# Kernel tuning notes

Measured on AMD Instinct MI355X. Metric: run time of the kernel, lower is better.

The kernel has to match this reference:

```python
import jax, jax.numpy as jnp
import numpy as np

N_QUBITS = 4
DEPTH = 2
B = 2048
IMG = 28
NUM_CLASSES = 2


def _apply_ry(state, theta, wire):
    # state: [N,2,2,2,2] complex64; RY(theta) on given wire (axis 1+wire)
    c = jnp.cos(theta / 2).astype(state.dtype)
    s = jnp.sin(theta / 2).astype(state.dtype)
    a0 = jnp.take(state, 0, axis=1 + wire)
    a1 = jnp.take(state, 1, axis=1 + wire)
    return jnp.stack([c * a0 - s * a1, s * a0 + c * a1], axis=1 + wire)


def _apply_crz(state, theta, control, target):
    # diagonal gate: multiply amplitudes with control bit = 1 by exp(+/- i theta/2)
    sc = [1, 1, 1, 1, 1]; sc[1 + control] = 2
    st = [1, 1, 1, 1, 1]; st[1 + target] = 2
    bc = jnp.arange(2).reshape(sc)
    bt = jnp.arange(2, dtype=jnp.float32).reshape(st)
    phase = jnp.exp((1j * (theta / 2) * (2.0 * bt - 1.0)).astype(state.dtype))
    return state * jnp.where(bc == 1, phase, jnp.ones((), state.dtype))


def _circuit(angles, ry_theta, crz_theta):
    # angles: [N,4]. Encoder resets to |0000> then RY(angle_k) on wire k ->
    # product state with per-wire amplitudes [cos(a/2), sin(a/2)].
    amp = jnp.stack([jnp.cos(angles / 2), jnp.sin(angles / 2)], axis=-1).astype(jnp.complex64)  # [N,4,2]
    state = jnp.einsum('na,nb,nc,nd->nabcd', amp[:, 0], amp[:, 1], amp[:, 2], amp[:, 3])
    for _ in range(DEPTH):
        for i in range(N_QUBITS):
            state = _apply_crz(state, crz_theta, i, (i + 1) % N_QUBITS)
        for j in range(N_QUBITS):
            state = _apply_ry(state, ry_theta, j)
    probs = jnp.real(state * jnp.conj(state))  # [N,2,2,2,2]
    sign = jnp.array([1.0, -1.0], dtype=probs.dtype)
    zs = [jnp.einsum('nabcd,' + 'abcd'[w] + '->n', probs, sign) for w in range(N_QUBITS)]
    return jnp.stack(zs, axis=-1)  # [N,4] PauliZ expectations, wire order 0..3


def _forward(x, ry_theta, crz_theta, fc1_w, fc1_b, fc2_w, fc2_b):
    ry_theta = ry_theta.reshape(())
    crz_theta = crz_theta.reshape(())
    b = x.shape[0]
    h = x.shape[2] // 2
    w = x.shape[3] // 2
    # stride-2 2x2 patches, row-major patch order, (di,dj) pixel order inside patch
    p = x.reshape(b, h, 2, w, 2).transpose(0, 1, 3, 2, 4).reshape(b * h * w, 4)
    z = _circuit(p, ry_theta, crz_theta).reshape(b, h * w * N_QUBITS)  # [B,784]
    hid = jax.nn.relu(z @ fc1_w.T + fc1_b)
    return hid @ fc2_w.T + fc2_b


def setup_inputs() -> dict:
    key = jax.random.key(0)
    ks = jax.random.split(key, 7)
    feat = N_QUBITS * (IMG // 2) * (IMG // 2)  # 784
    return {
        'x': jax.random.normal(ks[0], (B, 1, IMG, IMG), dtype=jnp.float32),
        'ry_theta': jax.random.normal(ks[1], (1,), dtype=jnp.float32),
        'crz_theta': jax.random.normal(ks[2], (1,), dtype=jnp.float32),
        'fc1_w': jax.random.normal(ks[3], (20, feat), dtype=jnp.float32) / np.sqrt(feat),
        'fc1_b': jax.random.normal(ks[4], (20,), dtype=jnp.float32) * 0.01,
        'fc2_w': jax.random.normal(ks[5], (NUM_CLASSES, 20), dtype=jnp.float32) / np.sqrt(20.0),
        'fc2_b': jax.random.normal(ks[6], (NUM_CLASSES,), dtype=jnp.float32) * 0.01,
    }


def reference(x, ry_theta, crz_theta, fc1_w, fc1_b, fc2_w, fc2_b):
    return _forward(x, ry_theta, crz_theta, fc1_w, fc1_b, fc2_w, fc2_b)
```

## Files before the change

kernel.cpp:

```cpp
#include <hip/hip_runtime.h>
#include <math.h>

#define NQ     4
#define IMGD   28
#define HP     14
#define NPATCH 196
#define BATCH  2048
#define FEAT   784
#define HID    20
#define NCLS   2
#define BTHR   320

__device__ __constant__ int d_ktab[16] = {0,-1,-1,0,-1,-2,0,1,-1,0,-2,1,0,1,1,4};


#define RYP(i,j)                                                    \
    { const float t0r = cr##i, t1r = cr##j;                         \
      const float t0i = ci##i, t1i = ci##j;                         \
      cr##i = cy * t0r - sy * t1r;  cr##j = sy * t0r + cy * t1r;    \
      ci##i = cy * t0i - sy * t1i;  ci##j = sy * t0i + cy * t1i; }

#define RY_LAYER()                                                  \
     RYP(0,8)  RYP(1,9)  RYP(2,10) RYP(3,11)     \
                       RYP(4,12) RYP(5,13) RYP(6,14) RYP(7,15)     \
     RYP(0,4)  RYP(1,5)  RYP(2,6)  RYP(3,7)      \
                       RYP(8,12) RYP(9,13) RYP(10,14) RYP(11,15)   \
     RYP(0,2)  RYP(1,3)  RYP(4,6)  RYP(5,7)      \
                       RYP(8,10) RYP(9,11) RYP(12,14) RYP(13,15)   \
     RYP(0,1)  RYP(2,3)  RYP(4,5)  RYP(6,7)      \
                       RYP(8,9)  RYP(10,11) RYP(12,13) RYP(14,15)

#define CRZC(i, c_, s_)                                             \
    { const float nr = cr##i * (c_) - ci##i * (s_);                 \
      ci##i = cr##i * (s_) + ci##i * (c_);  cr##i = nr; }

__global__ __launch_bounds__(256) void patch_z_kernel(
    const float* __restrict__ x,
    const float* __restrict__ ry_theta,
    const float* __restrict__ crz_theta,
    float* __restrict__ z)
{
    const int p  = blockIdx.x * 256 + threadIdx.x;
    const int b  = p / NPATCH;
    const int r  = p - b * NPATCH;
    const int ph = r / HP, pw = r - ph * HP;

    const float hcrz = 0.5f * crz_theta[0];
    const float c1 = __cosf(hcrz), s1 = __sinf(hcrz);
    const float c2 = c1 * c1 - s1 * s1, s2 = 2.f * c1 * s1;
    const float c4 = c2 * c2 - s2 * s2, s4 = 2.f * c2 * s2;
    const float hry = 0.5f * ry_theta[0];
    const float cy = __cosf(hry), sy = __sinf(hry);

    const float* xb = x + (size_t)b * (IMGD * IMGD);
    const float2 p0 = *(const float2*)(xb + (2 * ph)     * IMGD + 2 * pw);
    const float2 p1 = *(const float2*)(xb + (2 * ph + 1) * IMGD + 2 * pw);

    const float h0 = 0.5f * p0.x, h1 = 0.5f * p0.y;
    const float h2 = 0.5f * p1.x, h3 = 0.5f * p1.y;
    const float A0 = __cosf(h0), S0  = __sinf(h0);
    const float A1 = __cosf(h1), S1v = __sinf(h1);
    const float A2 = __cosf(h2), S2v = __sinf(h2);
    const float A3 = __cosf(h3), S3v = __sinf(h3);

    const float q00 = A0 * A1,  q01 = A0 * S1v, q10 = S0 * A1,  q11 = S0 * S1v;
    const float r00 = A2 * A3,  r01 = A2 * S3v, r10 = S2v * A3, r11 = S2v * S3v;
    float cr0  = q00 * r00, cr1  = q00 * r01, cr2  = q00 * r10, cr3  = q00 * r11;
    float cr4  = q01 * r00, cr5  = q01 * r01, cr6  = q01 * r10, cr7  = q01 * r11;
    float cr8  = q10 * r00, cr9  = q10 * r01, cr10 = q10 * r10, cr11 = q10 * r11;
    float cr12 = q11 * r00, cr13 = q11 * r01, cr14 = q11 * r10, cr15 = q11 * r11;

    float ci0 = 0.f, ci3 = 0.f, ci6 = 0.f, ci9 = 0.f, ci12 = 0.f;
    float ci1  = -cr1  * s1;  cr1  *= c1;
    float ci2  = -cr2  * s1;  cr2  *= c1;
    float ci4  = -cr4  * s1;  cr4  *= c1;
    float ci5  = -cr5  * s2;  cr5  *= c2;
    float ci7  =  cr7  * s1;  cr7  *= c1;
    float ci8  = -cr8  * s1;  cr8  *= c1;
    float ci10 = -cr10 * s2;  cr10 *= c2;
    float ci11 =  cr11 * s1;  cr11 *= c1;
    float ci13 =  cr13 * s1;  cr13 *= c1;
    float ci14 =  cr14 * s1;  cr14 *= c1;
    float ci15 =  cr15 * s4;  cr15 *= c4;

    RY_LAYER()

    CRZC(1,  c1, -s1)  CRZC(2,  c1, -s1)  CRZC(4,  c1, -s1)  CRZC(8,  c1, -s1)
    CRZC(5,  c2, -s2)  CRZC(10, c2, -s2)
    CRZC(7,  c1,  s1)  CRZC(11, c1,  s1)  CRZC(13, c1,  s1)  CRZC(14, c1,  s1)
    CRZC(15, c4,  s4)

    RY_LAYER()

#define PROB(i) const float pp##i = cr##i * cr##i + ci##i * ci##i;
    PROB(0) PROB(1) PROB(2) PROB(3) PROB(4) PROB(5) PROB(6) PROB(7)
    PROB(8) PROB(9) PROB(10) PROB(11) PROB(12) PROB(13) PROB(14) PROB(15)
#undef PROB
    const float t01 = pp0 + pp1,   t23 = pp2 + pp3;
    const float t45 = pp4 + pp5,   t67 = pp6 + pp7;
    const float t89 = pp8 + pp9,   tab = pp10 + pp11;
    const float tcd = pp12 + pp13, tef = pp14 + pp15;
    const float u0 = t01 + t23, u1 = t45 + t67, u2 = t89 + tab, u3 = tcd + tef;
    const float z0 = (u0 + u1) - (u2 + u3);
    const float z1 = (u0 + u2) - (u1 + u3);
    const float z2 = (t01 - t23) + (t45 - t67) + (t89 - tab) + (tcd - tef);
    const float z3 = ((pp0 - pp1) + (pp2 - pp3)) + ((pp4 - pp5) + (pp6 - pp7))
                   + ((pp8 - pp9) + (pp10 - pp11)) + ((pp12 - pp13) + (pp14 - pp15));

    *((float4*)&z[(size_t)p * 4]) = make_float4(z0, z1, z2, z3);
}

__global__ __launch_bounds__(BTHR) void fc_kernel(
    const float* __restrict__ z,
    const float* __restrict__ fc1_w,
    const float* __restrict__ fc1_b,
    const float* __restrict__ fc2_w,
    const float* __restrict__ fc2_b,
    float* __restrict__ out)
{
    __shared__ float zs[FEAT];
    __shared__ float hid_s[HID];

    const int tid = threadIdx.x;
    const int b   = blockIdx.x;

    if (tid < NPATCH)
        ((float4*)zs)[tid] = ((const float4*)(z + (size_t)b * FEAT))[tid];
    __syncthreads();

    const int g = tid >> 4;
    const int l = tid & 15;
    const float* wrow = fc1_w + g * FEAT;

    float4 a4 = make_float4(0.f, 0.f, 0.f, 0.f);
    const float4* z4 = (const float4*)zs;
    const float4* w4 = (const float4*)wrow;
    #pragma unroll
    for (int i = 0; i < 12; ++i) {
        const int f4 = l + (i << 4);
        const float4 zz = z4[f4];
        const float4 ww = w4[f4];
        a4.x += zz.x * ww.x;  a4.y += zz.y * ww.y;
        a4.z += zz.z * ww.z;  a4.w += zz.w * ww.w;
    }
    float acc = (a4.x + a4.y) + (a4.z + a4.w);
    acc += zs[768 + l] * wrow[768 + l];

    acc += __shfl_xor(acc, 1, 16);
    acc += __shfl_xor(acc, 2, 16);
    acc += __shfl_xor(acc, 4, 16);
    acc += __shfl_xor(acc, 8, 16);
    if (l == 0) hid_s[g] = acc + fc1_b[g];
    __syncthreads();

    if (tid < NCLS) {
        float o = fc2_b[tid];
        #pragma unroll
        for (int h = 0; h < HID; ++h)
            o += fmaxf(hid_s[h], 0.f) * fc2_w[tid * HID + h];
        out[b * NCLS + tid] = o;
    }
}

__global__ __launch_bounds__(256) void fused_qnn_kernel(
    const float* __restrict__ x, const float* __restrict__ ry_theta,
    const float* __restrict__ crz_theta, const float* __restrict__ fc1_w,
    const float* __restrict__ fc1_b, const float* __restrict__ fc2_w,
    const float* __restrict__ fc2_b, float* __restrict__ out)
{
    __shared__ float zs[FEAT];
    __shared__ float pc_s[16], ps_s[16];
    __shared__ float rycs[2];
    __shared__ float hid_s[HID];

    const int tid = threadIdx.x;
    const int b   = blockIdx.x;

    if (tid < 16) {
        float sv, cv;
        sincosf(0.5f * crz_theta[0] * (float)d_ktab[tid], &sv, &cv);
        pc_s[tid] = cv; ps_s[tid] = sv;
    } else if (tid == 16) {
        float sv, cv;
        sincosf(0.5f * ry_theta[0], &sv, &cv);
        rycs[0] = cv; rycs[1] = sv;
    }
    __syncthreads();

    if (tid < NPATCH) {
        const int ph = tid / HP, pw = tid % HP;
        const float* xb = x + (size_t)b * (IMGD * IMGD);
        const float2 p0 = *(const float2*)(xb + (2 * ph)     * IMGD + 2 * pw);
        const float2 p1 = *(const float2*)(xb + (2 * ph + 1) * IMGD + 2 * pw);
        const float ang[4] = {p0.x, p0.y, p1.x, p1.y};

        float Ac[4], As[4];
        #pragma unroll
        for (int k = 0; k < 4; ++k) { As[k] = __sinf(0.5f * ang[k]); Ac[k] = __cosf(0.5f * ang[k]); }

        float cr[16], ci[16];
        #pragma unroll
        for (int i = 0; i < 16; ++i) {
            cr[i] = ((i & 8) ? As[0] : Ac[0]) * ((i & 4) ? As[1] : Ac[1]) *
                    ((i & 2) ? As[2] : Ac[2]) * ((i & 1) ? As[3] : Ac[3]);
            ci[i] = 0.0f;
        }

        const float c = rycs[0], s = rycs[1];
        #pragma unroll
        for (int layer = 0; layer < 2; ++layer) {
            #pragma unroll
            for (int i = 0; i < 16; ++i) {
                const float pr = pc_s[i], pi = ps_s[i];
                const float nr = cr[i] * pr - ci[i] * pi;
                const float ni = cr[i] * pi + ci[i] * pr;
                cr[i] = nr; ci[i] = ni;
            }
            #pragma unroll
            for (int w = 0; w < 4; ++w) {
                const int m = 8 >> w;
                #pragma unroll
                for (int i = 0; i < 16; ++i) {
                    if (i & m) continue;
                    const int j = i | m;
                    const float a0r = cr[i], a1r = cr[j];
                    const float a0i = ci[i], a1i = ci[j];
                    cr[i] = c * a0r - s * a1r;
                    cr[j] = s * a0r + c * a1r;
                    ci[i] = c * a0i - s * a1i;
                    ci[j] = s * a0i + c * a1i;
                }
            }
        }

        float z0 = 0.f, z1 = 0.f, z2 = 0.f, z3 = 0.f;
        #pragma unroll
        for (int i = 0; i < 16; ++i) {
            const float pr = cr[i] * cr[i] + ci[i] * ci[i];
            z0 += (i & 8) ? -pr : pr;
            z1 += (i & 4) ? -pr : pr;
            z2 += (i & 2) ? -pr : pr;
            z3 += (i & 1) ? -pr : pr;
        }
        *((float4*)&zs[tid * 4]) = make_float4(z0, z1, z2, z3);
    }
    __syncthreads();

    const int wave = tid >> 6;
    const int lane = tid & 63;
    #pragma unroll
    for (int hh = 0; hh < 5; ++hh) {
        const int h = wave * 5 + hh;
        const float* wrow = fc1_w + h * FEAT;
        float acc = 0.f;
        #pragma unroll
        for (int f = lane; f < FEAT; f += 64)
            acc += zs[f] * wrow[f];
        #pragma unroll
        for (int off = 32; off > 0; off >>= 1)
            acc += __shfl_down(acc, off, 64);
        if (lane == 0) hid_s[h] = acc + fc1_b[h];
    }
    __syncthreads();

    if (tid < NCLS) {
        float acc = fc2_b[tid];
        #pragma unroll
        for (int h = 0; h < HID; ++h)
            acc += fmaxf(hid_s[h], 0.f) * fc2_w[tid * HID + h];
        out[b * NCLS + tid] = acc;
    }
}

extern "C" void kernel_launch(void* const* d_in, const int* in_sizes, int n_in,
                              void* d_out, int out_size, void* d_ws, size_t ws_size,
                              hipStream_t stream) {
    const float* x         = (const float*)d_in[0];
    const float* ry_theta  = (const float*)d_in[1];
    const float* crz_theta = (const float*)d_in[2];
    const float* fc1_w     = (const float*)d_in[3];
    const float* fc1_b     = (const float*)d_in[4];
    const float* fc2_w     = (const float*)d_in[5];
    const float* fc2_b     = (const float*)d_in[6];
    float* out = (float*)d_out;

    const size_t z_bytes = (size_t)BATCH * FEAT * sizeof(float);
    if (ws_size >= z_bytes) {
        float* z = (float*)d_ws;
        patch_z_kernel<<<(BATCH * NPATCH) / 256, 256, 0, stream>>>(
            x, ry_theta, crz_theta, z);
        fc_kernel<<<BATCH, BTHR, 0, stream>>>(z, fc1_w, fc1_b, fc2_w, fc2_b, out);
    } else {
        fused_qnn_kernel<<<BATCH, 256, 0, stream>>>(
            x, ry_theta, crz_theta, fc1_w, fc1_b, fc2_w, fc2_b, out);
    }
}
```

Measured before the change: 85.58 us.

## Fuse patch circuit and FC layers into one kernel per image

Replaces the two-kernel path (patch circuit writing z to workspace, then FC kernel reading it) with a single kernel per batch image. The optimized unrolled circuit code writes Z expectations straight into shared memory, and the 256-thread block then computes the 20 hidden units in two passes of 16-lane groups. This removes the global round trip of the 6.4 MB z buffer and one kernel launch. In exchange, only 196 of 256 threads do circuit work and the block is less parallel per image.

```diff
diff --git a/kernel.cpp b/kernel.cpp
--- a/kernel.cpp
+++ b/kernel.cpp
@@ -9,9 +9,6 @@
 #define FEAT   784
 #define HID    20
 #define NCLS   2
-#define BTHR   320
-
-__device__ __constant__ int d_ktab[16] = {0,-1,-1,0,-1,-2,0,1,-1,0,-2,1,0,1,1,4};
 
 
 #define RYP(i,j)                                                    \
@@ -34,84 +31,10 @@
     { const float nr = cr##i * (c_) - ci##i * (s_);                 \
       ci##i = cr##i * (s_) + ci##i * (c_);  cr##i = nr; }
 
-__global__ __launch_bounds__(256) void patch_z_kernel(
+__global__ __launch_bounds__(256) void fused_qnn_kernel(
     const float* __restrict__ x,
     const float* __restrict__ ry_theta,
     const float* __restrict__ crz_theta,
-    float* __restrict__ z)
-{
-    const int p  = blockIdx.x * 256 + threadIdx.x;
-    const int b  = p / NPATCH;
-    const int r  = p - b * NPATCH;
-    const int ph = r / HP, pw = r - ph * HP;
-
-    const float hcrz = 0.5f * crz_theta[0];
-    const float c1 = __cosf(hcrz), s1 = __sinf(hcrz);
-    const float c2 = c1 * c1 - s1 * s1, s2 = 2.f * c1 * s1;
-    const float c4 = c2 * c2 - s2 * s2, s4 = 2.f * c2 * s2;
-    const float hry = 0.5f * ry_theta[0];
-    const float cy = __cosf(hry), sy = __sinf(hry);
-
-    const float* xb = x + (size_t)b * (IMGD * IMGD);
-    const float2 p0 = *(const float2*)(xb + (2 * ph)     * IMGD + 2 * pw);
-    const float2 p1 = *(const float2*)(xb + (2 * ph + 1) * IMGD + 2 * pw);
-
-    const float h0 = 0.5f * p0.x, h1 = 0.5f * p0.y;
-    const float h2 = 0.5f * p1.x, h3 = 0.5f * p1.y;
-    const float A0 = __cosf(h0), S0  = __sinf(h0);
-    const float A1 = __cosf(h1), S1v = __sinf(h1);
-    const float A2 = __cosf(h2), S2v = __sinf(h2);
-    const float A3 = __cosf(h3), S3v = __sinf(h3);
-
-    const float q00 = A0 * A1,  q01 = A0 * S1v, q10 = S0 * A1,  q11 = S0 * S1v;
-    const float r00 = A2 * A3,  r01 = A2 * S3v, r10 = S2v * A3, r11 = S2v * S3v;
-    float cr0  = q00 * r00, cr1  = q00 * r01, cr2  = q00 * r10, cr3  = q00 * r11;
-    float cr4  = q01 * r00, cr5  = q01 * r01, cr6  = q01 * r10, cr7  = q01 * r11;
-    float cr8  = q10 * r00, cr9  = q10 * r01, cr10 = q10 * r10, cr11 = q10 * r11;
-    float cr12 = q11 * r00, cr13 = q11 * r01, cr14 = q11 * r10, cr15 = q11 * r11;
-
-    float ci0 = 0.f, ci3 = 0.f, ci6 = 0.f, ci9 = 0.f, ci12 = 0.f;
-    float ci1  = -cr1  * s1;  cr1  *= c1;
-    float ci2  = -cr2  * s1;  cr2  *= c1;
-    float ci4  = -cr4  * s1;  cr4  *= c1;
-    float ci5  = -cr5  * s2;  cr5  *= c2;
-    float ci7  =  cr7  * s1;  cr7  *= c1;
-    float ci8  = -cr8  * s1;  cr8  *= c1;
-    float ci10 = -cr10 * s2;  cr10 *= c2;
-    float ci11 =  cr11 * s1;  cr11 *= c1;
-    float ci13 =  cr13 * s1;  cr13 *= c1;
-    float ci14 =  cr14 * s1;  cr14 *= c1;
-    float ci15 =  cr15 * s4;  cr15 *= c4;
-
-    RY_LAYER()
-
-    CRZC(1,  c1, -s1)  CRZC(2,  c1, -s1)  CRZC(4,  c1, -s1)  CRZC(8,  c1, -s1)
-    CRZC(5,  c2, -s2)  CRZC(10, c2, -s2)
-    CRZC(7,  c1,  s1)  CRZC(11, c1,  s1)  CRZC(13, c1,  s1)  CRZC(14, c1,  s1)
-    CRZC(15, c4,  s4)
-
-    RY_LAYER()
-
-#define PROB(i) const float pp##i = cr##i * cr##i + ci##i * ci##i;
-    PROB(0) PROB(1) PROB(2) PROB(3) PROB(4) PROB(5) PROB(6) PROB(7)
-    PROB(8) PROB(9) PROB(10) PROB(11) PROB(12) PROB(13) PROB(14) PROB(15)
-#undef PROB
-    const float t01 = pp0 + pp1,   t23 = pp2 + pp3;
-    const float t45 = pp4 + pp5,   t67 = pp6 + pp7;
-    const float t89 = pp8 + pp9,   tab = pp10 + pp11;
-    const float tcd = pp12 + pp13, tef = pp14 + pp15;
-    const float u0 = t01 + t23, u1 = t45 + t67, u2 = t89 + tab, u3 = tcd + tef;
-    const float z0 = (u0 + u1) - (u2 + u3);
-    const float z1 = (u0 + u2) - (u1 + u3);
-    const float z2 = (t01 - t23) + (t45 - t67) + (t89 - tab) + (tcd - tef);
-    const float z3 = ((pp0 - pp1) + (pp2 - pp3)) + ((pp4 - pp5) + (pp6 - pp7))
-                   + ((pp8 - pp9) + (pp10 - pp11)) + ((pp12 - pp13) + (pp14 - pp15));
-
-    *((float4*)&z[(size_t)p * 4]) = make_float4(z0, z1, z2, z3);
-}
-
-__global__ __launch_bounds__(BTHR) void fc_kernel(
-    const float* __restrict__ z,
     const float* __restrict__ fc1_w,
     const float* __restrict__ fc1_b,
     const float* __restrict__ fc2_w,
@@ -124,33 +47,103 @@
     const int tid = threadIdx.x;
     const int b   = blockIdx.x;
 
-    if (tid < NPATCH)
-        ((float4*)zs)[tid] = ((const float4*)(z + (size_t)b * FEAT))[tid];
+    const float hcrz = 0.5f * crz_theta[0];
+    const float c1 = __cosf(hcrz), s1 = __sinf(hcrz);
+    const float c2 = c1 * c1 - s1 * s1, s2 = 2.f * c1 * s1;
+    const float c4 = c2 * c2 - s2 * s2, s4 = 2.f * c2 * s2;
+    const float hry = 0.5f * ry_theta[0];
+    const float cy = __cosf(hry), sy = __sinf(hry);
+
+    if (tid < NPATCH) {
+        const int ph = tid / HP, pw = tid - ph * HP;
+        const float* xb = x + (size_t)b * (IMGD * IMGD);
+        const float2 p0 = *(const float2*)(xb + (2 * ph)     * IMGD + 2 * pw);
+        const float2 p1 = *(const float2*)(xb + (2 * ph + 1) * IMGD + 2 * pw);
+
+        const float h0 = 0.5f * p0.x, h1 = 0.5f * p0.y;
+        const float h2 = 0.5f * p1.x, h3 = 0.5f * p1.y;
+        const float A0 = __cosf(h0), S0  = __sinf(h0);
+        const float A1 = __cosf(h1), S1v = __sinf(h1);
+        const float A2 = __cosf(h2), S2v = __sinf(h2);
+        const float A3 = __cosf(h3), S3v = __sinf(h3);
+
+        const float q00 = A0 * A1,  q01 = A0 * S1v, q10 = S0 * A1,  q11 = S0 * S1v;
+        const float r00 = A2 * A3,  r01 = A2 * S3v, r10 = S2v * A3, r11 = S2v * S3v;
+        float cr0  = q00 * r00, cr1  = q00 * r01, cr2  = q00 * r10, cr3  = q00 * r11;
+        float cr4  = q01 * r00, cr5  = q01 * r01, cr6  = q01 * r10, cr7  = q01 * r11;
+        float cr8  = q10 * r00, cr9  = q10 * r01, cr10 = q10 * r10, cr11 = q10 * r11;
+        float cr12 = q11 * r00, cr13 = q11 * r01, cr14 = q11 * r10, cr15 = q11 * r11;
+
+        float ci0 = 0.f, ci3 = 0.f, ci6 = 0.f, ci9 = 0.f, ci12 = 0.f;
+        float ci1  = -cr1  * s1;  cr1  *= c1;
+        float ci2  = -cr2  * s1;  cr2  *= c1;
+        float ci4  = -cr4  * s1;  cr4  *= c1;
+        float ci5  = -cr5  * s2;  cr5  *= c2;
+        float ci7  =  cr7  * s1;  cr7  *= c1;
+        float ci8  = -cr8  * s1;  cr8  *= c1;
+        float ci10 = -cr10 * s2;  cr10 *= c2;
+        float ci11 =  cr11 * s1;  cr11 *= c1;
+        float ci13 =  cr13 * s1;  cr13 *= c1;
+        float ci14 =  cr14 * s1;  cr14 *= c1;
+        float ci15 =  cr15 * s4;  cr15 *= c4;
+
+        RY_LAYER()
+
+        CRZC(1,  c1, -s1)  CRZC(2,  c1, -s1)  CRZC(4,  c1, -s1)  CRZC(8,  c1, -s1)
+        CRZC(5,  c2, -s2)  CRZC(10, c2, -s2)
+        CRZC(7,  c1,  s1)  CRZC(11, c1,  s1)  CRZC(13, c1,  s1)  CRZC(14, c1,  s1)
+        CRZC(15, c4,  s4)
+
+        RY_LAYER()
+
+#define PROB(i) const float pp##i = cr##i * cr##i + ci##i * ci##i;
+        PROB(0) PROB(1) PROB(2) PROB(3) PROB(4) PROB(5) PROB(6) PROB(7)
+        PROB(8) PROB(9) PROB(10) PROB(11) PROB(12) PROB(13) PROB(14) PROB(15)
+#undef PROB
+        const float t01 = pp0 + pp1,   t23 = pp2 + pp3;
+        const float t45 = pp4 + pp5,   t67 = pp6 + pp7;
+        const float t89 = pp8 + pp9,   tab = pp10 + pp11;
+        const float tcd = pp12 + pp13, tef = pp14 + pp15;
+        const float u0 = t01 + t23, u1 = t45 + t67, u2 = t89 + tab, u3 = tcd + tef;
+        const float z0 = (u0 + u1) - (u2 + u3);
+        const float z1 = (u0 + u2) - (u1 + u3);
+        const float z2 = (t01 - t23) + (t45 - t67) + (t89 - tab) + (tcd - tef);
+        const float z3 = ((pp0 - pp1) + (pp2 - pp3)) + ((pp4 - pp5) + (pp6 - pp7))
+                       + ((pp8 - pp9) + (pp10 - pp11)) + ((pp12 - pp13) + (pp14 - pp15));
+
+        *((float4*)&zs[tid * 4]) = make_float4(z0, z1, z2, z3);
+    }
     __syncthreads();
 
     const int g = tid >> 4;
     const int l = tid & 15;
-    const float* wrow = fc1_w + g * FEAT;
+    const float4* z4 = (const float4*)zs;
 
-    float4 a4 = make_float4(0.f, 0.f, 0.f, 0.f);
-    const float4* z4 = (const float4*)zs;
-    const float4* w4 = (const float4*)wrow;
     #pragma unroll
-    for (int i = 0; i < 12; ++i) {
-        const int f4 = l + (i << 4);
-        const float4 zz = z4[f4];
-        const float4 ww = w4[f4];
-        a4.x += zz.x * ww.x;  a4.y += zz.y * ww.y;
-        a4.z += zz.z * ww.z;  a4.w += zz.w * ww.w;
+    for (int pass = 0; pass < 2; ++pass) {
+        const int h = (pass == 0) ? g : (16 + g);
+        if (pass == 1 && g >= 4) break;
+        const float* wrow = fc1_w + h * FEAT;
+        const float4* w4 = (const float4*)wrow;
+
+        float4 a4 = make_float4(0.f, 0.f, 0.f, 0.f);
+        #pragma unroll
+        for (int i = 0; i < 12; ++i) {
+            const int f4 = l + (i << 4);
+            const float4 zz = z4[f4];
+            const float4 ww = w4[f4];
+            a4.x += zz.x * ww.x;  a4.y += zz.y * ww.y;
+            a4.z += zz.z * ww.z;  a4.w += zz.w * ww.w;
+        }
+        float acc = (a4.x + a4.y) + (a4.z + a4.w);
+        acc += zs[768 + l] * wrow[768 + l];
+
+        acc += __shfl_xor(acc, 1, 16);
+        acc += __shfl_xor(acc, 2, 16);
+        acc += __shfl_xor(acc, 4, 16);
+        acc += __shfl_xor(acc, 8, 16);
+        if (l == 0) hid_s[h] = acc + fc1_b[h];
     }
-    float acc = (a4.x + a4.y) + (a4.z + a4.w);
-    acc += zs[768 + l] * wrow[768 + l];
-
-    acc += __shfl_xor(acc, 1, 16);
-    acc += __shfl_xor(acc, 2, 16);
-    acc += __shfl_xor(acc, 4, 16);
-    acc += __shfl_xor(acc, 8, 16);
-    if (l == 0) hid_s[g] = acc + fc1_b[g];
     __syncthreads();
 
     if (tid < NCLS) {
@@ -159,116 +152,6 @@
         for (int h = 0; h < HID; ++h)
             o += fmaxf(hid_s[h], 0.f) * fc2_w[tid * HID + h];
         out[b * NCLS + tid] = o;
-    }
-}
-
-__global__ __launch_bounds__(256) void fused_qnn_kernel(
-    const float* __restrict__ x, const float* __restrict__ ry_theta,
-    const float* __restrict__ crz_theta, const float* __restrict__ fc1_w,
-    const float* __restrict__ fc1_b, const float* __restrict__ fc2_w,
-    const float* __restrict__ fc2_b, float* __restrict__ out)
-{
-    __shared__ float zs[FEAT];
-    __shared__ float pc_s[16], ps_s[16];
-    __shared__ float rycs[2];
-    __shared__ float hid_s[HID];
-
-    const int tid = threadIdx.x;
-    const int b   = blockIdx.x;
-
-    if (tid < 16) {
-        float sv, cv;
-        sincosf(0.5f * crz_theta[0] * (float)d_ktab[tid], &sv, &cv);
-        pc_s[tid] = cv; ps_s[tid] = sv;
-    } else if (tid == 16) {
-        float sv, cv;
-        sincosf(0.5f * ry_theta[0], &sv, &cv);
-        rycs[0] = cv; rycs[1] = sv;
-    }
-    __syncthreads();
-
-    if (tid < NPATCH) {
-        const int ph = tid / HP, pw = tid % HP;
-        const float* xb = x + (size_t)b * (IMGD * IMGD);
-        const float2 p0 = *(const float2*)(xb + (2 * ph)     * IMGD + 2 * pw);
-        const float2 p1 = *(const float2*)(xb + (2 * ph + 1) * IMGD + 2 * pw);
-        const float ang[4] = {p0.x, p0.y, p1.x, p1.y};
-
-        float Ac[4], As[4];
-        #pragma unroll
-        for (int k = 0; k < 4; ++k) { As[k] = __sinf(0.5f * ang[k]); Ac[k] = __cosf(0.5f * ang[k]); }
-
-        float cr[16], ci[16];
-        #pragma unroll
-        for (int i = 0; i < 16; ++i) {
-            cr[i] = ((i & 8) ? As[0] : Ac[0]) * ((i & 4) ? As[1] : Ac[1]) *
-                    ((i & 2) ? As[2] : Ac[2]) * ((i & 1) ? As[3] : Ac[3]);
-            ci[i] = 0.0f;
-        }
-
-        const float c = rycs[0], s = rycs[1];
-        #pragma unroll
-        for (int layer = 0; layer < 2; ++layer) {
-            #pragma unroll
-            for (int i = 0; i < 16; ++i) {
-                const float pr = pc_s[i], pi = ps_s[i];
-                const float nr = cr[i] * pr - ci[i] * pi;
-                const float ni = cr[i] * pi + ci[i] * pr;
-                cr[i] = nr; ci[i] = ni;
-            }
-            #pragma unroll
-            for (int w = 0; w < 4; ++w) {
-                const int m = 8 >> w;
-                #pragma unroll
-                for (int i = 0; i < 16; ++i) {
-                    if (i & m) continue;
-                    const int j = i | m;
-                    const float a0r = cr[i], a1r = cr[j];
-                    const float a0i = ci[i], a1i = ci[j];
-                    cr[i] = c * a0r - s * a1r;
-                    cr[j] = s * a0r + c * a1r;
-                    ci[i] = c * a0i - s * a1i;
-                    ci[j] = s * a0i + c * a1i;
-                }
-            }
-        }
-
-        float z0 = 0.f, z1 = 0.f, z2 = 0.f, z3 = 0.f;
-        #pragma unroll
-        for (int i = 0; i < 16; ++i) {
-            const float pr = cr[i] * cr[i] + ci[i] * ci[i];
-            z0 += (i & 8) ? -pr : pr;
-            z1 += (i & 4) ? -pr : pr;
-            z2 += (i & 2) ? -pr : pr;
-            z3 += (i & 1) ? -pr : pr;
-        }
-        *((float4*)&zs[tid * 4]) = make_float4(z0, z1, z2, z3);
-    }
-    __syncthreads();
-
-    const int wave = tid >> 6;
-    const int lane = tid & 63;
-    #pragma unroll
-    for (int hh = 0; hh < 5; ++hh) {
-        const int h = wave * 5 + hh;
-        const float* wrow = fc1_w + h * FEAT;
-        float acc = 0.f;
-        #pragma unroll
-        for (int f = lane; f < FEAT; f += 64)
-            acc += zs[f] * wrow[f];
-        #pragma unroll
-        for (int off = 32; off > 0; off >>= 1)
-            acc += __shfl_down(acc, off, 64);
-        if (lane == 0) hid_s[h] = acc + fc1_b[h];
-    }
-    __syncthreads();
-
-    if (tid < NCLS) {
-        float acc = fc2_b[tid];
-        #pragma unroll
-        for (int h = 0; h < HID; ++h)
-            acc += fmaxf(hid_s[h], 0.f) * fc2_w[tid * HID + h];
-        out[b * NCLS + tid] = acc;
     }
 }
 
@@ -284,14 +167,6 @@
     const float* fc2_b     = (const float*)d_in[6];
     float* out = (float*)d_out;
 
-    const size_t z_bytes = (size_t)BATCH * FEAT * sizeof(float);
-    if (ws_size >= z_bytes) {
-        float* z = (float*)d_ws;
-        patch_z_kernel<<<(BATCH * NPATCH) / 256, 256, 0, stream>>>(
-            x, ry_theta, crz_theta, z);
-        fc_kernel<<<BATCH, BTHR, 0, stream>>>(z, fc1_w, fc1_b, fc2_w, fc2_b, out);
-    } else {
-        fused_qnn_kernel<<<BATCH, 256, 0, stream>>>(
-            x, ry_theta, crz_theta, fc1_w, fc1_b, fc2_w, fc2_b, out);
-    }
+    fused_qnn_kernel<<<BATCH, 256, 0, stream>>>(
+        x, ry_theta, crz_theta, fc1_w, fc1_b, fc2_w, fc2_b, out);
 }
```

After: 79.88 us. 6.7% less time.
